# Optimization experiments

Measured on AMD Instinct MI355X. Metric: run time of the kernel, lower is better.

Reference implementation:

```python
import jax, jax.numpy as jnp
import numpy as np

B, C, H, W = 8, 256, 64, 64
CR = C // 8  # reduced channels = 32


def setup_inputs() -> dict:
    key = jax.random.key(0)
    k1, k2, k3, k4 = jax.random.split(key, 4)
    x = jax.random.normal(k1, (B, C, H, W), dtype=jnp.float32)
    # 1x1 conv weights (bias=False) are plain channel matmuls; scale like kaiming (~1/sqrt(fan_in))
    Wt = jax.random.normal(k2, (3 * CR, C), dtype=jnp.float32) * (1.0 / np.sqrt(C))
    Wo = jax.random.normal(k3, (C, CR), dtype=jnp.float32) * (1.0 / np.sqrt(CR))
    scale = jax.random.normal(k4, (1,), dtype=jnp.float32)
    return {"x": x, "Wt": Wt, "Wo": Wo, "scale": scale}


def reference(x, Wt, Wo, scale):
    b, c, h, w = x.shape
    n = h * w
    # 1x1 conv QKV projection: [B, 3*Cr, H, W]
    t = jnp.einsum('oc,bchw->bohw', Wt, x)
    cr = t.shape[1] // 3
    key = t[:, :cr].reshape(b, cr, n)          # [B, Cr, N]
    query = t[:, cr:2 * cr].reshape(b, cr, n)  # [B, Cr, N]
    value = t[:, 2 * cr:].reshape(b, cr, n)    # [B, Cr, N]
    # scores[b, i, j] = sum_c key[b,c,i] * query[b,c,j]  (key^T @ query)
    scores = jnp.einsum('bci,bcj->bij', key, query)  # [B, N, N]
    # torch Softmax(dim=1): normalize over the key axis i
    weights = jax.nn.softmax(scores, axis=1)
    # output[b, c, j] = sum_i value[b,c,i] * weights[b,i,j]
    out = jnp.einsum('bci,bij->bcj', value, weights)  # [B, Cr, N]
    out = out.reshape(b, cr, h, w)
    out = jnp.einsum('oc,bchw->bohw', Wo, out)  # 1x1 conv back to C channels
    return scale[0] * out + x
```

## Files before the change

### kernel.cpp

```cpp
#include <hip/hip_runtime.h>
#include <math.h>

#define B_ 8
#define C_ 256
#define CR_ 32
#define N_ 4096

typedef __attribute__((ext_vector_type(8))) short bf16x8;
typedef __attribute__((ext_vector_type(4))) short bf16x4;
typedef __attribute__((ext_vector_type(4))) float f32x4;
typedef __attribute__((ext_vector_type(16))) float f32x16;

__device__ inline short f2bf(float f) {
  union { float f; unsigned u; } v; v.f = f;
  unsigned r = v.u + 0x7FFFu + ((v.u >> 16) & 1u);
  return (short)(r >> 16);
}
__device__ inline float bf2f(short h) {
  union { unsigned u; float f; } v; v.u = ((unsigned)(unsigned short)h) << 16;
  return v.f;
}
__device__ inline short f2bf_r(float f) {
  return (short)((__float_as_uint(f) + 0x8000u) >> 16);
}

__global__ __launch_bounds__(256) void prep_weights(const float* __restrict__ Wt,
                                                    const float* __restrict__ Wo,
                                                    const float* __restrict__ scale,
                                                    short* __restrict__ WtHi,
                                                    short* __restrict__ WtLo,
                                                    short* __restrict__ WoB) {
  const int blk = blockIdx.x, tid = threadIdx.x;
  if (blk < 96) {
    float v = Wt[blk * C_ + tid];
    if (blk >= 32 && blk < 64) v *= 1.44269504f;
    const short h = f2bf(v);
    WtHi[blk * C_ + tid] = h;
    WtLo[blk * C_ + tid] = f2bf(v - bf2f(h));
  } else {
    const int idx = (blk - 96) * 256 + tid;
    WoB[idx] = f2bf(Wo[idx] * scale[0]);
  }
}

__global__ __launch_bounds__(256) void qkv_mfma(const float* __restrict__ x,
                                                const short* __restrict__ WtHi,
                                                const short* __restrict__ WtLo,
                                                short* __restrict__ t_tr,
                                                short* __restrict__ Vg) {
  const int b = blockIdx.y;
  const int tid = threadIdx.x;
  const int wave = tid >> 6, lane = tid & 63;
  const int col = lane & 15, quad = lane >> 4;
  const int n0 = (blockIdx.x * 4 + wave) * 16;

  const f32x4 z4 = {0.f, 0.f, 0.f, 0.f};
  f32x4 acc[6] = {z4, z4, z4, z4, z4, z4};

  const float* xb = x + (size_t)b * C_ * N_ + n0 + col;
  float xcur[8], xnxt[8];
#pragma unroll
  for (int j = 0; j < 8; ++j) xcur[j] = xb[(size_t)(quad * 8 + j) * N_];

#pragma unroll 2
  for (int c0 = 0; c0 < C_; c0 += 32) {
    if (c0 < C_ - 32) {
#pragma unroll
      for (int j = 0; j < 8; ++j)
        xnxt[j] = xb[(size_t)(c0 + 32 + quad * 8 + j) * N_];
    }
    bf16x8 xh, xl;
#pragma unroll
    for (int j = 0; j < 8; ++j) {
      const short h = (short)(__float_as_uint(xcur[j]) >> 16);
      xh[j] = h;
      xl[j] = f2bf_r(xcur[j] - bf2f(h));
    }
#pragma unroll
    for (int ot = 0; ot < 4; ++ot) {
      const int off = (ot * 16 + col) * C_ + c0 + quad * 8;
      const bf16x8 bh = *(const bf16x8*)(WtHi + off);
      const bf16x8 bl = *(const bf16x8*)(WtLo + off);
      acc[ot] = __builtin_amdgcn_mfma_f32_16x16x32_bf16(xh, bh, acc[ot], 0, 0, 0);
      acc[ot] = __builtin_amdgcn_mfma_f32_16x16x32_bf16(xl, bh, acc[ot], 0, 0, 0);
      acc[ot] = __builtin_amdgcn_mfma_f32_16x16x32_bf16(xh, bl, acc[ot], 0, 0, 0);
    }
#pragma unroll
    for (int ct = 0; ct < 2; ++ct) {
      const int off = ((64 + ct * 16) + col) * C_ + c0 + quad * 8;
      const bf16x8 ah = *(const bf16x8*)(WtHi + off);
      const bf16x8 al = *(const bf16x8*)(WtLo + off);
      acc[4 + ct] = __builtin_amdgcn_mfma_f32_16x16x32_bf16(ah, xh, acc[4 + ct], 0, 0, 0);
      acc[4 + ct] = __builtin_amdgcn_mfma_f32_16x16x32_bf16(ah, xl, acc[4 + ct], 0, 0, 0);
      acc[4 + ct] = __builtin_amdgcn_mfma_f32_16x16x32_bf16(al, xh, acc[4 + ct], 0, 0, 0);
    }
#pragma unroll
    for (int j = 0; j < 8; ++j) xcur[j] = xnxt[j];
  }
#pragma unroll
  for (int ot = 0; ot < 4; ++ot)
#pragma unroll
    for (int r = 0; r < 4; ++r)
      t_tr[((size_t)b * N_ + n0 + quad * 4 + r) * 64 + ot * 16 + col] =
          f2bf(acc[ot][r]);
#pragma unroll
  for (int ct = 0; ct < 2; ++ct)
#pragma unroll
    for (int r = 0; r < 4; ++r)
      Vg[(size_t)b * CR_ * N_ + (size_t)(ct * 16 + quad * 4 + r) * N_ + n0 + col] =
          f2bf(acc[4 + ct][r]);
}

__global__ __launch_bounds__(64, 2) void flash_attn(const short* __restrict__ t_tr,
                                                    const short* __restrict__ Vg,
                                                    short* __restrict__ OPart,
                                                    float* __restrict__ LPart) {
  const int b = blockIdx.z, hq = blockIdx.y;
  const int j0 = blockIdx.x * 64;
  const int lane = threadIdx.x;
  const int j32 = lane & 31, h32 = lane >> 5;
  const short* T = t_tr + (size_t)b * N_ * 64;
  const short* V = Vg + (size_t)b * CR_ * N_;

  const f32x16 z16 = {0.f};
  bf16x8 qf[2][2];
#pragma unroll
  for (int jt = 0; jt < 2; ++jt)
#pragma unroll
    for (int ch = 0; ch < 2; ++ch)
      qf[jt][ch] = *(const bf16x8*)(T + (size_t)(j0 + jt * 32 + j32) * 64 + 32 +
                                    ch * 16 + h32 * 8);

  f32x16 acc[2] = {z16, z16};
  float ps[2] = {0.f, 0.f};

  const int ibase = hq * 1024;
  bf16x8 kf[4], vf[4], kfn[4], vfn[4];
#pragma unroll
  for (int it = 0; it < 2; ++it)
#pragma unroll
    for (int ch = 0; ch < 2; ++ch)
      kf[it * 2 + ch] = *(const bf16x8*)(T + (size_t)(ibase + it * 32 + j32) * 64 +
                                         ch * 16 + h32 * 8);
#pragma unroll
  for (int ich = 0; ich < 4; ++ich)
    vf[ich] = *(const bf16x8*)(V + (size_t)j32 * N_ + ibase + ich * 16 + h32 * 8);

  for (int iter = 0; iter < 16; ++iter) {
    const int inx = ibase + ((iter + 1) & 15) * 64;
#pragma unroll
    for (int it = 0; it < 2; ++it)
#pragma unroll
      for (int ch = 0; ch < 2; ++ch)
        kfn[it * 2 + ch] = *(const bf16x8*)(T + (size_t)(inx + it * 32 + j32) * 64 +
                                            ch * 16 + h32 * 8);
#pragma unroll
    for (int ich = 0; ich < 4; ++ich)
      vfn[ich] = *(const bf16x8*)(V + (size_t)j32 * N_ + inx + ich * 16 + h32 * 8);

#pragma unroll
    for (int it = 0; it < 2; ++it) {
#pragma unroll
      for (int jt = 0; jt < 2; ++jt) {
        f32x16 s = __builtin_amdgcn_mfma_f32_32x32x16_bf16(kf[it * 2 + 0], qf[jt][0], z16, 0, 0, 0);
        s = __builtin_amdgcn_mfma_f32_32x32x16_bf16(kf[it * 2 + 1], qf[jt][1], s, 0, 0, 0);
        float p[16];
#pragma unroll
        for (int r = 0; r < 16; ++r) p[r] = __builtin_amdgcn_exp2f(s[r]);
        ps[jt] += (((p[0] + p[1]) + (p[2] + p[3])) + ((p[4] + p[5]) + (p[6] + p[7]))) +
                  (((p[8] + p[9]) + (p[10] + p[11])) + ((p[12] + p[13]) + (p[14] + p[15])));
        unsigned d[8], xw[8];
#pragma unroll
        for (int k = 0; k < 8; ++k) {
          const unsigned u0 = __float_as_uint(p[2 * k]) + 0x8000u;
          const unsigned u1 = __float_as_uint(p[2 * k + 1]) + 0x8000u;
          d[k] = __builtin_amdgcn_perm(u1, u0, 0x07060302u);
        }
#pragma unroll
        for (int k = 0; k < 8; ++k) xw[k] = __shfl_xor((int)d[k], 32);
        union { unsigned u[4]; bf16x8 v; } f0, f1;
        f0.u[0] = h32 ? xw[2] : d[0];
        f0.u[1] = h32 ? xw[3] : d[1];
        f0.u[2] = h32 ? d[2] : xw[0];
        f0.u[3] = h32 ? d[3] : xw[1];
        f1.u[0] = h32 ? xw[6] : d[4];
        f1.u[1] = h32 ? xw[7] : d[5];
        f1.u[2] = h32 ? d[6] : xw[4];
        f1.u[3] = h32 ? d[7] : xw[5];
        acc[jt] = __builtin_amdgcn_mfma_f32_32x32x16_bf16(vf[it * 2 + 0], f0.v, acc[jt], 0, 0, 0);
        acc[jt] = __builtin_amdgcn_mfma_f32_32x32x16_bf16(vf[it * 2 + 1], f1.v, acc[jt], 0, 0, 0);
      }
    }
#pragma unroll
    for (int k = 0; k < 4; ++k) { kf[k] = kfn[k]; vf[k] = vfn[k]; }
  }

  const size_t base = ((size_t)b * 4 + hq) * N_;
#pragma unroll
  for (int jt = 0; jt < 2; ++jt) {
    const float l = ps[jt] + __shfl_xor(ps[jt], 32);
    const int jg = j0 + jt * 32 + j32;
    if (h32 == 0) LPart[base + jg] = l;
    short* OP = OPart + (base + jg) * 32;
#pragma unroll
    for (int g = 0; g < 4; ++g) {
      bf16x4 o = {f2bf(acc[jt][4 * g + 0]), f2bf(acc[jt][4 * g + 1]),
                  f2bf(acc[jt][4 * g + 2]), f2bf(acc[jt][4 * g + 3])};
      *(bf16x4*)(OP + 8 * g + 4 * h32) = o;
    }
  }
}

__global__ __launch_bounds__(256) void out_proj(const short* __restrict__ OPart,
                                                const float* __restrict__ LPart,
                                                const short* __restrict__ WoB,
                                                const float* __restrict__ x,
                                                float* __restrict__ out) {
  const int b = blockIdx.z, chalf = blockIdx.y;
  const int tid = threadIdx.x;
  const int wave = tid >> 6, lane = tid & 63;
  const int col = lane & 15, quad = lane >> 4;
  const int jg = blockIdx.x * 64 + wave * 16 + col;
  const int n0 = blockIdx.x * 64 + wave * 16;

  float osum[8];
#pragma unroll
  for (int e = 0; e < 8; ++e) osum[e] = 0.f;
  float lsum = 0.f;
#pragma unroll
  for (int h = 0; h < 4; ++h) {
    const size_t p = ((size_t)b * 4 + h) * N_ + jg;
    const bf16x8 o = *(const bf16x8*)(OPart + p * 32 + quad * 8);
#pragma unroll
    for (int e = 0; e < 8; ++e) osum[e] += bf2f(o[e]);
    lsum += LPart[p];
  }
  const float linv = 1.f / lsum;
  bf16x8 bf;
#pragma unroll
  for (int e = 0; e < 8; ++e) bf[e] = f2bf(osum[e] * linv);

  const f32x4 z4 = {0.f, 0.f, 0.f, 0.f};
  const float* xb = x + (size_t)b * C_ * N_;
  float* ob = out + (size_t)b * C_ * N_;
#pragma unroll
  for (int ct = 0; ct < 8; ++ct) {
    const int ctg = chalf * 8 + ct;
    const bf16x8 af = *(const bf16x8*)(WoB + (ctg * 16 + col) * 32 + quad * 8);
    const f32x4 a = __builtin_amdgcn_mfma_f32_16x16x32_bf16(af, bf, z4, 0, 0, 0);
#pragma unroll
    for (int r = 0; r < 4; ++r) {
      const size_t idx = (size_t)(ctg * 16 + quad * 4 + r) * N_ + n0 + col;
      ob[idx] = a[r] + xb[idx];
    }
  }
}

extern "C" void kernel_launch(void* const* d_in, const int* in_sizes, int n_in,
                              void* d_out, int out_size, void* d_ws,
                              size_t ws_size, hipStream_t stream) {
  const float* x = (const float*)d_in[0];
  const float* Wt = (const float*)d_in[1];
  const float* Wo = (const float*)d_in[2];
  const float* scale = (const float*)d_in[3];
  float* out = (float*)d_out;

  short* OPart = (short*)d_ws;
  float* LPart = (float*)(OPart + (size_t)B_ * 4 * N_ * 32);
  short* t_tr = (short*)(LPart + (size_t)B_ * 4 * N_);
  short* Vg = t_tr + (size_t)B_ * N_ * 64;
  short* WtHi = Vg + (size_t)B_ * CR_ * N_;
  short* WtLo = WtHi + 96 * C_;
  short* WoB = WtLo + 96 * C_;

  prep_weights<<<dim3(128), 256, 0, stream>>>(Wt, Wo, scale, WtHi, WtLo, WoB);
  qkv_mfma<<<dim3(64, B_), 256, 0, stream>>>(x, WtHi, WtLo, t_tr, Vg);
  flash_attn<<<dim3(64, 4, B_), 64, 0, stream>>>(t_tr, Vg, OPart, LPart);
  out_proj<<<dim3(64, 2, B_), 256, 0, stream>>>(OPart, LPart, WoB, x, out);
}
```

Before: 156.6 us.

## Split attention key range into eight partitions and use permlane32 swap

```diff
diff --git a/kernel.cpp b/kernel.cpp
--- a/kernel.cpp
+++ b/kernel.cpp
@@ -5,11 +5,19 @@
 #define C_ 256
 #define CR_ 32
 #define N_ 4096
+#define NH_ 8
 
 typedef __attribute__((ext_vector_type(8))) short bf16x8;
 typedef __attribute__((ext_vector_type(4))) short bf16x4;
 typedef __attribute__((ext_vector_type(4))) float f32x4;
 typedef __attribute__((ext_vector_type(16))) float f32x16;
+typedef __attribute__((ext_vector_type(2))) unsigned uint32x2;
+
+#if defined(__has_builtin)
+#if __has_builtin(__builtin_amdgcn_permlane32_swap)
+#define HAVE_PLSWAP 1
+#endif
+#endif
 
 __device__ inline short f2bf(float f) {
   union { float f; unsigned u; } v; v.f = f;
@@ -111,7 +119,7 @@
           f2bf(acc[4 + ct][r]);
 }
 
-__global__ __launch_bounds__(64, 2) void flash_attn(const short* __restrict__ t_tr,
+__global__ __launch_bounds__(64, 4) void flash_attn(const short* __restrict__ t_tr,
                                                     const short* __restrict__ Vg,
                                                     short* __restrict__ OPart,
                                                     float* __restrict__ LPart) {
@@ -134,7 +142,7 @@
   f32x16 acc[2] = {z16, z16};
   float ps[2] = {0.f, 0.f};
 
-  const int ibase = hq * 1024;
+  const int ibase = hq * 512;
   bf16x8 kf[4], vf[4], kfn[4], vfn[4];
 #pragma unroll
   for (int it = 0; it < 2; ++it)
@@ -146,8 +154,8 @@
   for (int ich = 0; ich < 4; ++ich)
     vf[ich] = *(const bf16x8*)(V + (size_t)j32 * N_ + ibase + ich * 16 + h32 * 8);
 
-  for (int iter = 0; iter < 16; ++iter) {
-    const int inx = ibase + ((iter + 1) & 15) * 64;
+  for (int iter = 0; iter < 8; ++iter) {
+    const int inx = ibase + ((iter + 1) & 7) * 64;
 #pragma unroll
     for (int it = 0; it < 2; ++it)
 #pragma unroll
@@ -162,40 +170,60 @@
     for (int it = 0; it < 2; ++it) {
 #pragma unroll
       for (int jt = 0; jt < 2; ++jt) {
+        __builtin_amdgcn_s_setprio(1);
         f32x16 s = __builtin_amdgcn_mfma_f32_32x32x16_bf16(kf[it * 2 + 0], qf[jt][0], z16, 0, 0, 0);
         s = __builtin_amdgcn_mfma_f32_32x32x16_bf16(kf[it * 2 + 1], qf[jt][1], s, 0, 0, 0);
+        __builtin_amdgcn_s_setprio(0);
         float p[16];
 #pragma unroll
         for (int r = 0; r < 16; ++r) p[r] = __builtin_amdgcn_exp2f(s[r]);
         ps[jt] += (((p[0] + p[1]) + (p[2] + p[3])) + ((p[4] + p[5]) + (p[6] + p[7]))) +
                   (((p[8] + p[9]) + (p[10] + p[11])) + ((p[12] + p[13]) + (p[14] + p[15])));
-        unsigned d[8], xw[8];
+        unsigned d[8];
 #pragma unroll
         for (int k = 0; k < 8; ++k) {
           const unsigned u0 = __float_as_uint(p[2 * k]) + 0x8000u;
           const unsigned u1 = __float_as_uint(p[2 * k + 1]) + 0x8000u;
           d[k] = __builtin_amdgcn_perm(u1, u0, 0x07060302u);
         }
-#pragma unroll
-        for (int k = 0; k < 8; ++k) xw[k] = __shfl_xor((int)d[k], 32);
         union { unsigned u[4]; bf16x8 v; } f0, f1;
-        f0.u[0] = h32 ? xw[2] : d[0];
-        f0.u[1] = h32 ? xw[3] : d[1];
-        f0.u[2] = h32 ? d[2] : xw[0];
-        f0.u[3] = h32 ? d[3] : xw[1];
-        f1.u[0] = h32 ? xw[6] : d[4];
-        f1.u[1] = h32 ? xw[7] : d[5];
-        f1.u[2] = h32 ? d[6] : xw[4];
-        f1.u[3] = h32 ? d[7] : xw[5];
+#ifdef HAVE_PLSWAP
+        {
+          const uint32x2 r0 = __builtin_amdgcn_permlane32_swap(d[0], d[2], false, false);
+          f0.u[0] = r0[0]; f0.u[2] = r0[1];
+          const uint32x2 r1 = __builtin_amdgcn_permlane32_swap(d[1], d[3], false, false);
+          f0.u[1] = r1[0]; f0.u[3] = r1[1];
+          const uint32x2 r2 = __builtin_amdgcn_permlane32_swap(d[4], d[6], false, false);
+          f1.u[0] = r2[0]; f1.u[2] = r2[1];
+          const uint32x2 r3 = __builtin_amdgcn_permlane32_swap(d[5], d[7], false, false);
+          f1.u[1] = r3[0]; f1.u[3] = r3[1];
+        }
+#else
+        {
+          unsigned xw[8];
+#pragma unroll
+          for (int k = 0; k < 8; ++k) xw[k] = __shfl_xor((int)d[k], 32);
+          f0.u[0] = h32 ? xw[2] : d[0];
+          f0.u[1] = h32 ? xw[3] : d[1];
+          f0.u[2] = h32 ? d[2] : xw[0];
+          f0.u[3] = h32 ? d[3] : xw[1];
+          f1.u[0] = h32 ? xw[6] : d[4];
+          f1.u[1] = h32 ? xw[7] : d[5];
+          f1.u[2] = h32 ? d[6] : xw[4];
+          f1.u[3] = h32 ? d[7] : xw[5];
+        }
+#endif
+        __builtin_amdgcn_s_setprio(1);
         acc[jt] = __builtin_amdgcn_mfma_f32_32x32x16_bf16(vf[it * 2 + 0], f0.v, acc[jt], 0, 0, 0);
         acc[jt] = __builtin_amdgcn_mfma_f32_32x32x16_bf16(vf[it * 2 + 1], f1.v, acc[jt], 0, 0, 0);
+        __builtin_amdgcn_s_setprio(0);
       }
     }
 #pragma unroll
     for (int k = 0; k < 4; ++k) { kf[k] = kfn[k]; vf[k] = vfn[k]; }
   }
 
-  const size_t base = ((size_t)b * 4 + hq) * N_;
+  const size_t base = ((size_t)b * NH_ + hq) * N_;
 #pragma unroll
   for (int jt = 0; jt < 2; ++jt) {
     const float l = ps[jt] + __shfl_xor(ps[jt], 32);
@@ -228,8 +256,8 @@
   for (int e = 0; e < 8; ++e) osum[e] = 0.f;
   float lsum = 0.f;
 #pragma unroll
-  for (int h = 0; h < 4; ++h) {
-    const size_t p = ((size_t)b * 4 + h) * N_ + jg;
+  for (int h = 0; h < NH_; ++h) {
+    const size_t p = ((size_t)b * NH_ + h) * N_ + jg;
     const bf16x8 o = *(const bf16x8*)(OPart + p * 32 + quad * 8);
 #pragma unroll
     for (int e = 0; e < 8; ++e) osum[e] += bf2f(o[e]);
@@ -266,8 +294,8 @@
   float* out = (float*)d_out;
 
   short* OPart = (short*)d_ws;
-  float* LPart = (float*)(OPart + (size_t)B_ * 4 * N_ * 32);
-  short* t_tr = (short*)(LPart + (size_t)B_ * 4 * N_);
+  float* LPart = (float*)(OPart + (size_t)B_ * NH_ * N_ * 32);
+  short* t_tr = (short*)(LPart + (size_t)B_ * NH_ * N_);
   short* Vg = t_tr + (size_t)B_ * N_ * 64;
   short* WtHi = Vg + (size_t)B_ * CR_ * N_;
   short* WtLo = WtHi + 96 * C_;
@@ -275,6 +303,6 @@
 
   prep_weights<<<dim3(128), 256, 0, stream>>>(Wt, Wo, scale, WtHi, WtLo, WoB);
   qkv_mfma<<<dim3(64, B_), 256, 0, stream>>>(x, WtHi, WtLo, t_tr, Vg);
-  flash_attn<<<dim3(64, 4, B_), 64, 0, stream>>>(t_tr, Vg, OPart, LPart);
+  flash_attn<<<dim3(64, NH_, B_), 64, 0, stream>>>(t_tr, Vg, OPart, LPart);
   out_proj<<<dim3(64, 2, B_), 256, 0, stream>>>(OPart, LPart, WoB, x, out);
 }
```

Result: slower. 286.2 us (+82.7%).
